# Kernel tuning notes

Measured on AMD Instinct MI355X. Metric: run time of the kernel, lower is better.

The kernel has to match this reference:

```python
import jax, jax.numpy as jnp
import numpy as np

NUM_BREAKPOINTS = 100  # module default
IMG_SHAPE = (1, 1, 4096, 8192)  # B must be 1: PWL(num_channels=1) sees (C*H*W, B)


def setup_inputs() -> dict:
    key = jax.random.key(0)
    k1, k2, k3, k4 = jax.random.split(key, 4)
    x = jax.random.uniform(k1, IMG_SHAPE, dtype=jnp.float32)
    # torchpwl.PWL parameters (num_channels=1): breakpoint x-positions, per-segment
    # slopes, and bias (function value at the leftmost breakpoint).
    x_positions = jax.random.uniform(k2, (1, NUM_BREAKPOINTS), dtype=jnp.float32)
    slopes = 1.0 + 0.1 * jax.random.normal(k3, (1, NUM_BREAKPOINTS), dtype=jnp.float32)
    biases = 0.05 * jax.random.normal(k4, (1,), dtype=jnp.float32)
    return {"x": x, "x_positions": x_positions, "slopes": slopes, "biases": biases}


def _pwl(x_flat, x_positions, slopes, biases):
    # Sloped piecewise-linear function (torchpwl.BaseSlopedPWL math), 1 channel.
    # x_flat: (N,), x_positions/slopes: (1, K), biases: (1,)
    K = x_positions.shape[1]
    sorted_x = jnp.sort(x_positions, axis=1)                     # (1, K)
    skips = jnp.roll(sorted_x, -1, axis=1) - sorted_x            # last entry never used
    cumsums = jnp.cumsum(skips * slopes, axis=1)[:, :-1]         # (1, K-1)
    betas = jnp.concatenate([biases[:, None], biases[:, None] + cumsums], axis=1)  # (1, K)
    # segment index: (# breakpoints <= x) clamped to [1, K], minus 1
    idx = jnp.clip(jnp.searchsorted(sorted_x[0], x_flat, side="right"), 1, K) - 1
    return betas[0, idx] + (x_flat - sorted_x[0, idx]) * slopes[0, idx]


def reference(x, x_positions, slopes, biases):
    # forward: flatten -> PWL -> clip(0,1) -> reshape (original returns [out])
    y = _pwl(x.reshape(-1), x_positions, slopes, biases)
    return jnp.clip(y, 0.0, 1.0).reshape(x.shape)
```

## Files before the change

### kernel.cpp

```cpp
#include <hip/hip_runtime.h>

#define K  100
#define NB 1024

typedef float fvec4 __attribute__((ext_vector_type(4)));

__global__ __launch_bounds__(1024) void pwl_setup_kernel(
    const float* __restrict__ xp, const float* __restrict__ sl,
    const float* __restrict__ bias, unsigned int* __restrict__ lut_g,
    float* __restrict__ sx_g, float2* __restrict__ ab_g) {
  __shared__ float s_pos[K];
  __shared__ float s_slope[K];
  __shared__ float s_sorted[K];
  __shared__ float s_beta[K];
  __shared__ unsigned short s_cnt[NB + 1];
  const int t = threadIdx.x;

  if (t < K) { s_pos[t] = xp[t]; s_slope[t] = sl[t]; }
  __syncthreads();

  if (t < K) {
    float v = s_pos[t];
    int r = 0;
    for (int j = 0; j < K; ++j) {
      float u = s_pos[j];
      r += ((u < v) || (u == v && j < t)) ? 1 : 0;
    }
    s_sorted[r] = v;
  }
  __syncthreads();

  if (t == 0) {
    float acc = bias[0];
    s_beta[0] = acc;
    for (int i = 1; i < K; ++i) {
      acc = acc + (s_sorted[i] - s_sorted[i - 1]) * s_slope[i - 1];
      s_beta[i] = acc;
    }
  }
  __syncthreads();

  if (t < K) {
    float a = s_slope[t];
    float b = s_beta[t] - s_sorted[t] * a;
    sx_g[t] = s_sorted[t];
    ab_g[t] = make_float2(a, b);
  }

  for (int e = t; e <= NB; e += blockDim.x) {
    float ev = (float)e * (1.0f / (float)NB);
    int c = 0;
    for (int j = 0; j < K; ++j) c += (s_sorted[j] <= ev) ? 1 : 0;
    s_cnt[e] = (unsigned short)c;
  }
  __syncthreads();

  for (int b = t; b < NB; b += blockDim.x) {
    lut_g[b] = (unsigned int)s_cnt[b] | ((unsigned int)s_cnt[b + 1] << 16);
  }
}

__device__ __forceinline__ float pwl_eval(float xv,
                                          const unsigned int* __restrict__ s_lut,
                                          const float* __restrict__ s_x,
                                          const float2* __restrict__ s_ab) {
  int b = (int)(xv * (float)NB);
  b = min(max(b, 0), NB - 1);
  unsigned int p = s_lut[b];
  int lo = (int)(p & 0xffffu);
  int hi = (int)(p >> 16);
  while (lo < hi) {
    int mid = (lo + hi) >> 1;
    if (s_x[mid] <= xv) lo = mid + 1; else hi = mid;
  }
  int idx = min(max(lo, 1), K) - 1;
  float2 ab = s_ab[idx];
  float y = fmaf(xv, ab.x, ab.y);
  return fminf(fmaxf(y, 0.0f), 1.0f);
}

__global__ __launch_bounds__(256) void pwl_main_kernel(
    const fvec4* __restrict__ x, const unsigned int* __restrict__ lut_g,
    const float* __restrict__ sx_g, const float2* __restrict__ ab_g,
    fvec4* __restrict__ out, int n4, int n) {
  __shared__ unsigned int s_lut[NB];
  __shared__ float s_x[K];
  __shared__ float2 s_ab[K];
  for (int i = threadIdx.x; i < NB; i += blockDim.x) s_lut[i] = lut_g[i];
  if (threadIdx.x < K) {
    s_x[threadIdx.x] = sx_g[threadIdx.x];
    s_ab[threadIdx.x] = ab_g[threadIdx.x];
  }
  __syncthreads();

  const int stride = gridDim.x * blockDim.x;
  for (int i = blockIdx.x * blockDim.x + threadIdx.x; i < n4; i += stride) {
    fvec4 v = __builtin_nontemporal_load(&x[i]);
    fvec4 r;
    r.x = pwl_eval(v.x, s_lut, s_x, s_ab);
    r.y = pwl_eval(v.y, s_lut, s_x, s_ab);
    r.z = pwl_eval(v.z, s_lut, s_x, s_ab);
    r.w = pwl_eval(v.w, s_lut, s_x, s_ab);
    __builtin_nontemporal_store(r, &out[i]);
  }

  if (blockIdx.x == 0) {
    const float* xs = (const float*)x;
    float* os = (float*)out;
    for (int i = (n4 << 2) + threadIdx.x; i < n; i += blockDim.x) {
      os[i] = pwl_eval(xs[i], s_lut, s_x, s_ab);
    }
  }
}

extern "C" void kernel_launch(void* const* d_in, const int* in_sizes, int n_in,
                              void* d_out, int out_size, void* d_ws, size_t ws_size,
                              hipStream_t stream) {
  const float* x    = (const float*)d_in[0];
  const float* xp   = (const float*)d_in[1];
  const float* sl   = (const float*)d_in[2];
  const float* bias = (const float*)d_in[3];
  float* out = (float*)d_out;

  unsigned int* lut = (unsigned int*)d_ws;
  float* sx         = (float*)((char*)d_ws + NB * 4);
  float2* ab        = (float2*)((char*)d_ws + NB * 4 + 512);

  const int n  = in_sizes[0];
  const int n4 = n >> 2;

  pwl_setup_kernel<<<1, 1024, 0, stream>>>(xp, sl, bias, lut, sx, ab);

  const int threads = 256;
  const int blocks  = 2048;
  pwl_main_kernel<<<blocks, threads, 0, stream>>>(
      (const fvec4*)x, lut, sx, ab, (fvec4*)out, n4, n);
}
```

Baseline: 236.6 us.

## Store direct slope/intercept in LUT buckets with one breakpoint; prefetch next vector

```diff
diff --git a/kernel.cpp b/kernel.cpp
--- a/kernel.cpp
+++ b/kernel.cpp
@@ -7,12 +7,13 @@
 
 __global__ __launch_bounds__(1024) void pwl_setup_kernel(
     const float* __restrict__ xp, const float* __restrict__ sl,
-    const float* __restrict__ bias, unsigned int* __restrict__ lut_g,
+    const float* __restrict__ bias, float2* __restrict__ bab_g,
     float* __restrict__ sx_g, float2* __restrict__ ab_g) {
   __shared__ float s_pos[K];
   __shared__ float s_slope[K];
   __shared__ float s_sorted[K];
-  __shared__ float s_beta[K];
+  __shared__ float s_a[K];
+  __shared__ float s_b[K];
   __shared__ unsigned short s_cnt[NB + 1];
   const int t = threadIdx.x;
 
@@ -32,19 +33,18 @@
 
   if (t == 0) {
     float acc = bias[0];
-    s_beta[0] = acc;
-    for (int i = 1; i < K; ++i) {
-      acc = acc + (s_sorted[i] - s_sorted[i - 1]) * s_slope[i - 1];
-      s_beta[i] = acc;
+    for (int i = 0; i < K; ++i) {
+      if (i) acc += (s_sorted[i] - s_sorted[i - 1]) * s_slope[i - 1];
+      float a = s_slope[i];
+      s_a[i] = a;
+      s_b[i] = acc - s_sorted[i] * a;
     }
   }
   __syncthreads();
 
   if (t < K) {
-    float a = s_slope[t];
-    float b = s_beta[t] - s_sorted[t] * a;
     sx_g[t] = s_sorted[t];
-    ab_g[t] = make_float2(a, b);
+    ab_g[t] = make_float2(s_a[t], s_b[t]);
   }
 
   for (int e = t; e <= NB; e += blockDim.x) {
@@ -56,37 +56,49 @@
   __syncthreads();
 
   for (int b = t; b < NB; b += blockDim.x) {
-    lut_g[b] = (unsigned int)s_cnt[b] | ((unsigned int)s_cnt[b + 1] << 16);
+    int lo = s_cnt[b], hi = s_cnt[b + 1];
+    float2 e;
+    if (lo == hi) {
+      int idx = min(max(lo, 1), K) - 1;
+      e = make_float2(s_a[idx], s_b[idx]);
+    } else {
+      e.x = __builtin_huge_valf();
+      e.y = __uint_as_float((unsigned)lo | ((unsigned)hi << 16));
+    }
+    bab_g[b] = e;
   }
 }
 
 __device__ __forceinline__ float pwl_eval(float xv,
-                                          const unsigned int* __restrict__ s_lut,
+                                          const float2* __restrict__ s_bab,
                                           const float* __restrict__ s_x,
                                           const float2* __restrict__ s_ab) {
   int b = (int)(xv * (float)NB);
   b = min(max(b, 0), NB - 1);
-  unsigned int p = s_lut[b];
-  int lo = (int)(p & 0xffffu);
-  int hi = (int)(p >> 16);
-  while (lo < hi) {
-    int mid = (lo + hi) >> 1;
-    if (s_x[mid] <= xv) lo = mid + 1; else hi = mid;
+  float2 ab = s_bab[b];
+  if (__float_as_uint(ab.x) == 0x7f800000u) {
+    unsigned p = __float_as_uint(ab.y);
+    int lo = (int)(p & 0xffffu);
+    int hi = (int)(p >> 16);
+    while (lo < hi) {
+      int mid = (lo + hi) >> 1;
+      if (s_x[mid] <= xv) lo = mid + 1; else hi = mid;
+    }
+    int idx = min(max(lo, 1), K) - 1;
+    ab = s_ab[idx];
   }
-  int idx = min(max(lo, 1), K) - 1;
-  float2 ab = s_ab[idx];
   float y = fmaf(xv, ab.x, ab.y);
   return fminf(fmaxf(y, 0.0f), 1.0f);
 }
 
 __global__ __launch_bounds__(256) void pwl_main_kernel(
-    const fvec4* __restrict__ x, const unsigned int* __restrict__ lut_g,
+    const fvec4* __restrict__ x, const float2* __restrict__ bab_g,
     const float* __restrict__ sx_g, const float2* __restrict__ ab_g,
     fvec4* __restrict__ out, int n4, int n) {
-  __shared__ unsigned int s_lut[NB];
+  __shared__ float2 s_bab[NB];
   __shared__ float s_x[K];
   __shared__ float2 s_ab[K];
-  for (int i = threadIdx.x; i < NB; i += blockDim.x) s_lut[i] = lut_g[i];
+  for (int i = threadIdx.x; i < NB; i += blockDim.x) s_bab[i] = bab_g[i];
   if (threadIdx.x < K) {
     s_x[threadIdx.x] = sx_g[threadIdx.x];
     s_ab[threadIdx.x] = ab_g[threadIdx.x];
@@ -94,21 +106,31 @@
   __syncthreads();
 
   const int stride = gridDim.x * blockDim.x;
-  for (int i = blockIdx.x * blockDim.x + threadIdx.x; i < n4; i += stride) {
+  int i = blockIdx.x * blockDim.x + threadIdx.x;
+  if (i < n4) {
     fvec4 v = __builtin_nontemporal_load(&x[i]);
-    fvec4 r;
-    r.x = pwl_eval(v.x, s_lut, s_x, s_ab);
-    r.y = pwl_eval(v.y, s_lut, s_x, s_ab);
-    r.z = pwl_eval(v.z, s_lut, s_x, s_ab);
-    r.w = pwl_eval(v.w, s_lut, s_x, s_ab);
-    __builtin_nontemporal_store(r, &out[i]);
+    while (true) {
+      int inext = i + stride;
+      bool more = inext < n4;
+      fvec4 vn = {};
+      if (more) vn = __builtin_nontemporal_load(&x[inext]);
+      fvec4 r;
+      r.x = pwl_eval(v.x, s_bab, s_x, s_ab);
+      r.y = pwl_eval(v.y, s_bab, s_x, s_ab);
+      r.z = pwl_eval(v.z, s_bab, s_x, s_ab);
+      r.w = pwl_eval(v.w, s_bab, s_x, s_ab);
+      __builtin_nontemporal_store(r, &out[i]);
+      if (!more) break;
+      v = vn;
+      i = inext;
+    }
   }
 
   if (blockIdx.x == 0) {
     const float* xs = (const float*)x;
     float* os = (float*)out;
-    for (int i = (n4 << 2) + threadIdx.x; i < n; i += blockDim.x) {
-      os[i] = pwl_eval(xs[i], s_lut, s_x, s_ab);
+    for (int j = (n4 << 2) + threadIdx.x; j < n; j += blockDim.x) {
+      os[j] = pwl_eval(xs[j], s_bab, s_x, s_ab);
     }
   }
 }
@@ -122,17 +144,17 @@
   const float* bias = (const float*)d_in[3];
   float* out = (float*)d_out;
 
-  unsigned int* lut = (unsigned int*)d_ws;
-  float* sx         = (float*)((char*)d_ws + NB * 4);
-  float2* ab        = (float2*)((char*)d_ws + NB * 4 + 512);
+  float2* bab = (float2*)d_ws;
+  float* sx   = (float*)((char*)d_ws + NB * 8);
+  float2* ab  = (float2*)((char*)d_ws + NB * 8 + 512);
 
   const int n  = in_sizes[0];
   const int n4 = n >> 2;
 
-  pwl_setup_kernel<<<1, 1024, 0, stream>>>(xp, sl, bias, lut, sx, ab);
+  pwl_setup_kernel<<<1, 1024, 0, stream>>>(xp, sl, bias, bab, sx, ab);
 
   const int threads = 256;
   const int blocks  = 2048;
   pwl_main_kernel<<<blocks, threads, 0, stream>>>(
-      (const fvec4*)x, lut, sx, ab, (fvec4*)out, n4, n);
+      (const fvec4*)x, bab, sx, ab, (fvec4*)out, n4, n);
 }
```

Result: no change. 236.5 us (-0.0%).
